# Optimization experiments

Measured on AMD Instinct MI355X. Metric: run time of the kernel, lower is better.

Reference implementation:

```python
import jax, jax.numpy as jnp
import numpy as np

B, S, D = 2, 2048, 768
H, STRIDE = 12, 8
HD = D // H  # 64


def setup_inputs() -> dict:
    key = jax.random.key(0)
    k0, k1, k2 = jax.random.split(key, 3)
    x = jax.random.normal(k0, (B, S, D), dtype=jnp.float32)
    qkv_w = jax.random.normal(k1, (3 * D, D), dtype=jnp.float32) * 0.02
    qkv_b = jnp.zeros((3 * D,), dtype=jnp.float32)
    out_w = jax.random.normal(k2, (D, D), dtype=jnp.float32) * 0.02
    out_b = jnp.zeros((D,), dtype=jnp.float32)
    return {"x": x, "qkv_w": qkv_w, "qkv_b": qkv_b, "out_w": out_w, "out_b": out_b}


def _stride_mask(S, stride, causal):
    i = jnp.arange(S)[:, None]
    j = jnp.arange(S)[None, :]
    strided = (j % stride == 0)
    if causal:
        strided = strided & (j <= i)
    # diagonal always attended; previous token attended for i > 0
    return strided | (j == i) | (j == i - 1)


def reference(x, qkv_w, qkv_b, out_w, out_b):
    Bx, Sx, Dx = x.shape
    qkv = x @ qkv_w.T + qkv_b                      # [B,S,3D]
    qkv = qkv.reshape(Bx, Sx, 3, H, HD)
    q, k, v = jnp.transpose(qkv, (2, 0, 3, 1, 4))  # each [B,H,S,HD]
    scale = HD ** -0.5
    attn = jnp.einsum('bhid,bhjd->bhij', q, k) * scale  # [B,H,S,S]
    mask = _stride_mask(Sx, STRIDE, True)          # [S,S] bool
    attn = jnp.where(mask[None, None], attn, -jnp.inf)
    a = jax.nn.softmax(attn, axis=-1)
    # every row has at least the diagonal unmasked, so no NaN rows;
    # nan_to_num kept for exact parity with the torch module
    a = jnp.nan_to_num(a, nan=0.0)
    out = jnp.einsum('bhij,bhjd->bhid', a, v)      # [B,H,S,HD]
    out = jnp.transpose(out, (0, 2, 1, 3)).reshape(Bx, Sx, Dx)
    return out @ out_w.T + out_b
```

## Files before the change

### kernel.cpp

```cpp
#include <hip/hip_runtime.h>
#include <hip/hip_bf16.h>
#include <stdint.h>

#define H_   12
#define S_   2048
#define D_   768
#define HD_  64
#define MS_  256

typedef __bf16 bf16_8 __attribute__((ext_vector_type(8)));
typedef float  f32_4  __attribute__((ext_vector_type(4)));

typedef __attribute__((address_space(1))) void* gas_ptr;
typedef __attribute__((address_space(3))) void* las_ptr;

__device__ __forceinline__ void g2l16(const void* g, void* l) {
  __builtin_amdgcn_global_load_lds((gas_ptr)g, (las_ptr)l, 16, 0, 0);
}

__device__ __forceinline__ f32_4 mfma16(bf16_8 a, bf16_8 b, f32_4 c) {
  return __builtin_amdgcn_mfma_f32_16x16x32_bf16(a, b, c, 0, 0, 0);
}

__device__ __forceinline__ bf16_8 ld8(const __hip_bfloat16* p) {
  return *reinterpret_cast<const bf16_8*>(p);
}

__global__ __launch_bounds__(256) void cvt3_f32_bf16(
    const float* __restrict__ a, const float* __restrict__ b,
    const float* __restrict__ c, __hip_bfloat16* __restrict__ out,
    int na4, int nb4) {
  const int t = blockIdx.x * 256 + threadIdx.x;
  float4 f;
  if (t < na4)            f = reinterpret_cast<const float4*>(a)[t];
  else if (t < na4 + nb4) f = reinterpret_cast<const float4*>(b)[t - na4];
  else                    f = reinterpret_cast<const float4*>(c)[t - na4 - nb4];
  union { __hip_bfloat16 h[4]; ushort4 u; } p;
  p.h[0] = __float2bfloat16(f.x);
  p.h[1] = __float2bfloat16(f.y);
  p.h[2] = __float2bfloat16(f.z);
  p.h[3] = __float2bfloat16(f.w);
  reinterpret_cast<ushort4*>(out)[t] = p.u;
}

template <int MODE, int BN>
__global__ __launch_bounds__(256, 2) void gemm_bt(
    const __hip_bfloat16* __restrict__ A, const __hip_bfloat16* __restrict__ B,
    const float* __restrict__ bias,
    __hip_bfloat16* __restrict__ O0, __hip_bfloat16* __restrict__ O1,
    __hip_bfloat16* __restrict__ O2, __hip_bfloat16* __restrict__ O3,
    __hip_bfloat16* __restrict__ O4, float* __restrict__ OF,
    int M, int N, int K) {
  constexpr int NTJ = BN / 32;
  __shared__ __bf16 sA[128 * 32];
  __shared__ __bf16 sB[BN * 32];
  const int tid  = threadIdx.x;
  const int lane = tid & 63;
  const int wv   = tid >> 6;
  const int m0 = blockIdx.y * 128;
  const int n0 = blockIdx.x * BN;
  const int wr = (wv >> 1) * 64;
  const int wc = (wv & 1) * (BN / 2);

  f32_4 acc[4][NTJ] = {};

  const __hip_bfloat16* aS = A + (size_t)(m0 + (tid >> 2)) * K + ((tid & 3) << 3);
  const __hip_bfloat16* bS = B + (size_t)(n0 + (tid >> 2)) * K + ((tid & 3) << 3);
  const size_t half = (size_t)64 * K;
  __bf16* dA  = &sA[tid * 8];
  __bf16* dA2 = &sA[tid * 8 + 2048];
  __bf16* dB  = &sB[tid * 8];
  __bf16* dB2 = &sB[tid * 8 + 2048];

  const int fr = lane & 15;
  const int kq = (lane >> 4) << 3;

  for (int k0 = 0; k0 < K; k0 += 32) {
    g2l16(aS, dA);
    g2l16(aS + half, dA2);
    g2l16(bS, dB);
    if constexpr (BN == 128) g2l16(bS + half, dB2);
    aS += 32;
    bS += 32;
    __syncthreads();
    bf16_8 af[4], bfm[NTJ];
#pragma unroll
    for (int t = 0; t < 4; ++t)
      af[t] = *reinterpret_cast<const bf16_8*>(&sA[(wr + t * 16 + fr) * 32 + kq]);
#pragma unroll
    for (int t = 0; t < NTJ; ++t)
      bfm[t] = *reinterpret_cast<const bf16_8*>(&sB[(wc + t * 16 + fr) * 32 + kq]);
#pragma unroll
    for (int ti = 0; ti < 4; ++ti)
#pragma unroll
      for (int tj = 0; tj < NTJ; ++tj)
        acc[ti][tj] = mfma16(af[ti], bfm[tj], acc[ti][tj]);
    __syncthreads();
  }

  const int crow = (lane >> 4) << 2;
  const int ccol = lane & 15;
#pragma unroll
  for (int ti = 0; ti < 4; ++ti) {
    const int gmb = m0 + wr + ti * 16 + crow;
#pragma unroll
    for (int tj = 0; tj < NTJ; ++tj) {
      const int gn = n0 + wc + tj * 16 + ccol;
      const float bv = bias[gn];
      if (MODE == 0) {
        const int t   = gn / D_;
        const int rem = gn - t * D_;
        const int hh = rem >> 6, dd = rem & 63;
        __hip_bfloat16* dst = (t == 0) ? O0 : (t == 1) ? O1 : O2;
#pragma unroll
        for (int r = 0; r < 4; ++r) {
          const int gm = gmb + r;
          const int bb = gm >> 11, ss = gm & (S_ - 1);
          const __hip_bfloat16 hv = __float2bfloat16(acc[ti][tj][r] + bv);
          dst[(((size_t)(bb * H_ + hh) << 11) + ss) * HD_ + dd] = hv;
          if (r == 0 && (gmb & 7) == 0) {
            if (t == 1)
              O4[(((size_t)(bb * H_ + hh)) * MS_ + (ss >> 3)) * HD_ + dd] = hv;
            else if (t == 2)
              O3[((size_t)(bb * H_ + hh) * HD_ + dd) * MS_ + (ss >> 3)] = hv;
          }
        }
      } else {
#pragma unroll
        for (int r = 0; r < 4; ++r)
          OF[(size_t)(gmb + r) * D_ + gn] = acc[ti][tj][r] + bv;
      }
    }
  }
}

__global__ __launch_bounds__(256) void attn_mfma(
    const __hip_bfloat16* __restrict__ Q, const __hip_bfloat16* __restrict__ Kb,
    const __hip_bfloat16* __restrict__ Ks, const __hip_bfloat16* __restrict__ Vr,
    const __hip_bfloat16* __restrict__ VsT, __hip_bfloat16* __restrict__ ctx) {
  __shared__ __bf16 pt[4][16 * 40];
  __shared__ __bf16 vb[4][32 * 64];
  const int lane = threadIdx.x & 63;
  const int wv   = threadIdx.x >> 6;
  const int task = blockIdx.x * 4 + wv;
  const int bh   = task >> 7;
  const int i0   = (task & 127) << 4;
  const int lr   = lane & 15;
  const int quad = lane >> 4;
  const float SC = 0.125f * 1.44269504088896340736f;

  const __hip_bfloat16* Kh  = Kb  + ((size_t)bh << 11) * HD_;
  const __hip_bfloat16* Ksh = Ks  + (size_t)bh * MS_ * HD_;
  const __hip_bfloat16* Vrh = Vr  + ((size_t)bh << 11) * HD_;
  const __hip_bfloat16* Vsh = VsT + (size_t)bh * HD_ * MS_;
  __bf16* ptw = pt[wv];
  __bf16* vbw = vb[wv];

  const int jbase = (i0 >= 8) ? (i0 - 8) : 0;

#pragma unroll
  for (int it = 0; it < 4; ++it) {
    const int cidx = it * 64 + lane;
    const int row = cidx >> 3, seg = cidx & 7;
    const int j  = jbase + row;
    const int jr = (j < S_) ? j : (S_ - 1);
    *reinterpret_cast<bf16_8*>(vbw + row * 64 + seg * 8) =
        ld8(Vrh + (size_t)jr * HD_ + seg * 8);
  }
  bf16_8 kb_[2][2];
#pragma unroll
  for (int t = 0; t < 2; ++t) {
    const int j  = jbase + t * 16 + lr;
    const int jr = (j < S_) ? j : (S_ - 1);
    const __hip_bfloat16* kp = Kh + (size_t)jr * HD_ + quad * 8;
    kb_[t][0] = ld8(kp);
    kb_[t][1] = ld8(kp + 32);
  }

  const __hip_bfloat16* qp = Q + (((size_t)bh << 11) + i0 + lr) * HD_ + quad * 8;
  const bf16_8 qf0 = ld8(qp);
  const bf16_8 qf1 = ld8(qp + 32);

  const __bf16 one = (__bf16)1.0f;
  const bf16_8 onesf = {one, one, one, one, one, one, one, one};

  f32_4 Lacc = {}, oacc[4];
#pragma unroll
  for (int ct = 0; ct < 4; ++ct) oacc[ct] = f32_4{0.f, 0.f, 0.f, 0.f};

  const int mmax = (i0 + 15) >> 3;
  const int nstr = (mmax >> 5) + 1;

  auto load_str = [&](int c, bf16_8 (&kf)[2][2], bf16_8 (&vf)[4]) {
    const int mb = c << 5;
#pragma unroll
    for (int t = 0; t < 2; ++t) {
      const __hip_bfloat16* kp = Ksh + (size_t)(mb + t * 16 + lr) * HD_ + quad * 8;
      kf[t][0] = ld8(kp);
      kf[t][1] = ld8(kp + 32);
    }
#pragma unroll
    for (int ct = 0; ct < 4; ++ct)
      vf[ct] = ld8(Vsh + (size_t)(ct * 16 + lr) * MS_ + mb + quad * 8);
  };

  auto softmax_pv = [&](f32_4& s0, f32_4& s1, const bf16_8 (&vf)[4]) {
#pragma unroll
    for (int r = 0; r < 4; ++r) {
      const int row = quad * 4 + r;
      ptw[row * 40 + lr]      = (__bf16)__float2bfloat16(s0[r]);
      ptw[row * 40 + 16 + lr] = (__bf16)__float2bfloat16(s1[r]);
    }
    const bf16_8 pf = *reinterpret_cast<const bf16_8*>(&ptw[lr * 40 + quad * 8]);
#pragma unroll
    for (int ct = 0; ct < 4; ++ct) oacc[ct] = mfma16(pf, vf[ct], oacc[ct]);
    Lacc = mfma16(pf, onesf, Lacc);
  };

  bf16_8 kf[2][2], vf[4], kf2[2][2], vf2[4];
  load_str(0, kf, vf);
  for (int c = 0; c < nstr; ++c) {
    const bool more = (c + 1 < nstr);
    if (more) load_str(c + 1, kf2, vf2);
    const int mb = c << 5;

    f32_4 s0 = {}, s1 = {};
    s0 = mfma16(qf0, kf[0][0], s0);
    s0 = mfma16(qf1, kf[0][1], s0);
    s1 = mfma16(qf0, kf[1][0], s1);
    s1 = mfma16(qf1, kf[1][1], s1);

#pragma unroll
    for (int r = 0; r < 4; ++r) {
      const int i = i0 + quad * 4 + r;
      const bool v0 = ((mb + lr) << 3) <= i;
      const bool v1 = ((mb + 16 + lr) << 3) <= i;
      s0[r] = v0 ? exp2f(fminf(s0[r] * SC, 63.f)) : 0.f;
      s1[r] = v1 ? exp2f(fminf(s1[r] * SC, 63.f)) : 0.f;
    }
    softmax_pv(s0, s1, vf);

    if (more) {
#pragma unroll
      for (int t = 0; t < 2; ++t) { kf[t][0] = kf2[t][0]; kf[t][1] = kf2[t][1]; }
#pragma unroll
      for (int ct = 0; ct < 4; ++ct) vf[ct] = vf2[ct];
    }
  }

  {
    f32_4 s0 = {}, s1 = {};
    s0 = mfma16(qf0, kb_[0][0], s0);
    s0 = mfma16(qf1, kb_[0][1], s0);
    s1 = mfma16(qf0, kb_[1][0], s1);
    s1 = mfma16(qf1, kb_[1][1], s1);

#pragma unroll
    for (int r = 0; r < 4; ++r) {
      const int i = i0 + quad * 4 + r;
      const int j0 = jbase + lr, j1 = jbase + 16 + lr;
      const bool v0 = (j0 == i || j0 == i - 1) && (j0 & 7);
      const bool v1 = (j1 == i || j1 == i - 1) && (j1 & 7);
      s0[r] = v0 ? exp2f(fminf(s0[r] * SC, 63.f)) : 0.f;
      s1[r] = v1 ? exp2f(fminf(s1[r] * SC, 63.f)) : 0.f;
    }

    bf16_8 vfb[4];
#pragma unroll
    for (int ct = 0; ct < 4; ++ct) {
      bf16_8 tmp;
#pragma unroll
      for (int e = 0; e < 8; ++e)
        tmp[e] = vbw[(quad * 8 + e) * 64 + ct * 16 + lr];
      vfb[ct] = tmp;
    }
    softmax_pv(s0, s1, vfb);
  }

  const int b = bh / H_;
  const int h = bh - b * H_;
  f32_4 inv;
#pragma unroll
  for (int r = 0; r < 4; ++r) inv[r] = 1.f / Lacc[r];
#pragma unroll
  for (int r = 0; r < 4; ++r) {
    const int i = i0 + quad * 4 + r;
    __hip_bfloat16* cp = ctx + ((size_t)(b * S_ + i)) * D_ + h * HD_ + lr;
#pragma unroll
    for (int ct = 0; ct < 4; ++ct)
      cp[ct * 16] = __float2bfloat16(oacc[ct][r] * inv[r]);
  }
}

extern "C" void kernel_launch(void* const* d_in, const int* in_sizes, int n_in,
                              void* d_out, int out_size, void* d_ws, size_t ws_size,
                              hipStream_t stream) {
  const float* x    = (const float*)d_in[0];
  const float* qkvw = (const float*)d_in[1];
  const float* qkvb = (const float*)d_in[2];
  const float* outw = (const float*)d_in[3];
  const float* outb = (const float*)d_in[4];
  float* out = (float*)d_out;

  const size_t NX  = (size_t)2 * S_ * D_;
  const size_t NW1 = (size_t)3 * D_ * D_;
  const size_t NW2 = (size_t)D_ * D_;
  const size_t NVS = (size_t)2 * H_ * HD_ * MS_;

  __hip_bfloat16* xb  = (__hip_bfloat16*)d_ws;
  __hip_bfloat16* w1b = xb + NX;
  __hip_bfloat16* w2b = w1b + NW1;
  __hip_bfloat16* q   = w2b + NW2;
  __hip_bfloat16* k   = q + NX;
  __hip_bfloat16* vr  = k + NX;
  __hip_bfloat16* vst = vr + NX;
  __hip_bfloat16* ks  = vst + NVS;
  __hip_bfloat16* ctx = ks + NVS;

  const int na4 = (int)(NX / 4), nb4 = (int)(NW1 / 4), nc4 = (int)(NW2 / 4);
  cvt3_f32_bf16<<<dim3((na4 + nb4 + nc4) / 256), 256, 0, stream>>>(
      x, qkvw, outw, xb, na4, nb4);

  gemm_bt<0, 128><<<dim3(2304 / 128, 4096 / 128), 256, 0, stream>>>(
      xb, w1b, qkvb, q, k, vr, vst, ks, nullptr, 4096, 2304, 768);

  attn_mfma<<<dim3(2 * H_ * S_ / 16 / 4), 256, 0, stream>>>(q, k, ks, vr, vst, ctx);

  gemm_bt<1, 64><<<dim3(768 / 64, 4096 / 128), 256, 0, stream>>>(
      ctx, w2b, outb, nullptr, nullptr, nullptr, nullptr, nullptr,
      out, 4096, 768, 768);
}
```

Before: 150.1 us.

## Fuse output projection into attention kernel with one block per 16-row tile

Attention now runs one 768-thread block per 16 query rows, with one wavefront per head. Each head writes its context slice into shared memory, and the block then computes the 16x768 output projection directly, so the ctx round-trip and the separate output GEMM launch disappear. The V tile is loaded straight into registers with scalar gathers instead of being staged through LDS. In exchange, each block streams the full W2 from global/L2 with no reuse across M tiles (only 16 rows per block). The grid also shrinks to 256 large blocks, which may hurt occupancy.

```diff
diff --git a/kernel.cpp b/kernel.cpp
--- a/kernel.cpp
+++ b/kernel.cpp
@@ -43,26 +43,23 @@
   reinterpret_cast<ushort4*>(out)[t] = p.u;
 }
 
-template <int MODE, int BN>
-__global__ __launch_bounds__(256, 2) void gemm_bt(
+__global__ __launch_bounds__(256, 2) void gemm_qkv(
     const __hip_bfloat16* __restrict__ A, const __hip_bfloat16* __restrict__ B,
     const float* __restrict__ bias,
     __hip_bfloat16* __restrict__ O0, __hip_bfloat16* __restrict__ O1,
     __hip_bfloat16* __restrict__ O2, __hip_bfloat16* __restrict__ O3,
-    __hip_bfloat16* __restrict__ O4, float* __restrict__ OF,
-    int M, int N, int K) {
-  constexpr int NTJ = BN / 32;
+    __hip_bfloat16* __restrict__ O4, int K) {
   __shared__ __bf16 sA[128 * 32];
-  __shared__ __bf16 sB[BN * 32];
+  __shared__ __bf16 sB[128 * 32];
   const int tid  = threadIdx.x;
   const int lane = tid & 63;
   const int wv   = tid >> 6;
   const int m0 = blockIdx.y * 128;
-  const int n0 = blockIdx.x * BN;
+  const int n0 = blockIdx.x * 128;
   const int wr = (wv >> 1) * 64;
-  const int wc = (wv & 1) * (BN / 2);
-
-  f32_4 acc[4][NTJ] = {};
+  const int wc = (wv & 1) * 64;
+
+  f32_4 acc[4][4] = {};
 
   const __hip_bfloat16* aS = A + (size_t)(m0 + (tid >> 2)) * K + ((tid & 3) << 3);
   const __hip_bfloat16* bS = B + (size_t)(n0 + (tid >> 2)) * K + ((tid & 3) << 3);
@@ -79,21 +76,21 @@
     g2l16(aS, dA);
     g2l16(aS + half, dA2);
     g2l16(bS, dB);
-    if constexpr (BN == 128) g2l16(bS + half, dB2);
+    g2l16(bS + half, dB2);
     aS += 32;
     bS += 32;
     __syncthreads();
-    bf16_8 af[4], bfm[NTJ];
+    bf16_8 af[4], bfm[4];
 #pragma unroll
     for (int t = 0; t < 4; ++t)
       af[t] = *reinterpret_cast<const bf16_8*>(&sA[(wr + t * 16 + fr) * 32 + kq]);
 #pragma unroll
-    for (int t = 0; t < NTJ; ++t)
+    for (int t = 0; t < 4; ++t)
       bfm[t] = *reinterpret_cast<const bf16_8*>(&sB[(wc + t * 16 + fr) * 32 + kq]);
 #pragma unroll
     for (int ti = 0; ti < 4; ++ti)
 #pragma unroll
-      for (int tj = 0; tj < NTJ; ++tj)
+      for (int tj = 0; tj < 4; ++tj)
         acc[ti][tj] = mfma16(af[ti], bfm[tj], acc[ti][tj]);
     __syncthreads();
   }
@@ -104,47 +101,43 @@
   for (int ti = 0; ti < 4; ++ti) {
     const int gmb = m0 + wr + ti * 16 + crow;
 #pragma unroll
-    for (int tj = 0; tj < NTJ; ++tj) {
+    for (int tj = 0; tj < 4; ++tj) {
       const int gn = n0 + wc + tj * 16 + ccol;
       const float bv = bias[gn];
-      if (MODE == 0) {
-        const int t   = gn / D_;
-        const int rem = gn - t * D_;
-        const int hh = rem >> 6, dd = rem & 63;
-        __hip_bfloat16* dst = (t == 0) ? O0 : (t == 1) ? O1 : O2;
-#pragma unroll
-        for (int r = 0; r < 4; ++r) {
-          const int gm = gmb + r;
-          const int bb = gm >> 11, ss = gm & (S_ - 1);
-          const __hip_bfloat16 hv = __float2bfloat16(acc[ti][tj][r] + bv);
-          dst[(((size_t)(bb * H_ + hh) << 11) + ss) * HD_ + dd] = hv;
-          if (r == 0 && (gmb & 7) == 0) {
-            if (t == 1)
-              O4[(((size_t)(bb * H_ + hh)) * MS_ + (ss >> 3)) * HD_ + dd] = hv;
-            else if (t == 2)
-              O3[((size_t)(bb * H_ + hh) * HD_ + dd) * MS_ + (ss >> 3)] = hv;
-          }
+      const int t   = gn / D_;
+      const int rem = gn - t * D_;
+      const int hh = rem >> 6, dd = rem & 63;
+      __hip_bfloat16* dst = (t == 0) ? O0 : (t == 1) ? O1 : O2;
+#pragma unroll
+      for (int r = 0; r < 4; ++r) {
+        const int gm = gmb + r;
+        const int bb = gm >> 11, ss = gm & (S_ - 1);
+        const __hip_bfloat16 hv = __float2bfloat16(acc[ti][tj][r] + bv);
+        dst[(((size_t)(bb * H_ + hh) << 11) + ss) * HD_ + dd] = hv;
+        if (r == 0 && (gmb & 7) == 0) {
+          if (t == 1)
+            O4[(((size_t)(bb * H_ + hh)) * MS_ + (ss >> 3)) * HD_ + dd] = hv;
+          else if (t == 2)
+            O3[((size_t)(bb * H_ + hh) * HD_ + dd) * MS_ + (ss >> 3)] = hv;
         }
-      } else {
-#pragma unroll
-        for (int r = 0; r < 4; ++r)
-          OF[(size_t)(gmb + r) * D_ + gn] = acc[ti][tj][r] + bv;
       }
     }
   }
 }
 
-__global__ __launch_bounds__(256) void attn_mfma(
+__global__ __launch_bounds__(768) void attn_out(
     const __hip_bfloat16* __restrict__ Q, const __hip_bfloat16* __restrict__ Kb,
     const __hip_bfloat16* __restrict__ Ks, const __hip_bfloat16* __restrict__ Vr,
-    const __hip_bfloat16* __restrict__ VsT, __hip_bfloat16* __restrict__ ctx) {
-  __shared__ __bf16 pt[4][16 * 40];
-  __shared__ __bf16 vb[4][32 * 64];
+    const __hip_bfloat16* __restrict__ VsT, const __hip_bfloat16* __restrict__ W2,
+    const float* __restrict__ b2, float* __restrict__ out) {
+  __shared__ __bf16 pt[12][16 * 40];
+  __shared__ __bf16 cx[16][776];
   const int lane = threadIdx.x & 63;
-  const int wv   = threadIdx.x >> 6;
-  const int task = blockIdx.x * 4 + wv;
-  const int bh   = task >> 7;
+  const int h    = threadIdx.x >> 6;
+  const int task = blockIdx.x;
+  const int b    = task >> 7;
   const int i0   = (task & 127) << 4;
+  const int bh   = b * H_ + h;
   const int lr   = lane & 15;
   const int quad = lane >> 4;
   const float SC = 0.125f * 1.44269504088896340736f;
@@ -153,20 +146,20 @@
   const __hip_bfloat16* Ksh = Ks  + (size_t)bh * MS_ * HD_;
   const __hip_bfloat16* Vrh = Vr  + ((size_t)bh << 11) * HD_;
   const __hip_bfloat16* Vsh = VsT + (size_t)bh * HD_ * MS_;
-  __bf16* ptw = pt[wv];
-  __bf16* vbw = vb[wv];
+  __bf16* ptw = pt[h];
 
   const int jbase = (i0 >= 8) ? (i0 - 8) : 0;
 
-#pragma unroll
-  for (int it = 0; it < 4; ++it) {
-    const int cidx = it * 64 + lane;
-    const int row = cidx >> 3, seg = cidx & 7;
-    const int j  = jbase + row;
-    const int jr = (j < S_) ? j : (S_ - 1);
-    *reinterpret_cast<bf16_8*>(vbw + row * 64 + seg * 8) =
-        ld8(Vrh + (size_t)jr * HD_ + seg * 8);
-  }
+  const __bf16* Vrb = reinterpret_cast<const __bf16*>(Vrh);
+  bf16_8 vfb[4];
+#pragma unroll
+  for (int ct = 0; ct < 4; ++ct)
+#pragma unroll
+    for (int e = 0; e < 8; ++e) {
+      const int j  = jbase + quad * 8 + e;
+      const int jr = (j < S_) ? j : (S_ - 1);
+      vfb[ct][e] = Vrb[(size_t)jr * HD_ + ct * 16 + lr];
+    }
   bf16_8 kb_[2][2];
 #pragma unroll
   for (int t = 0; t < 2; ++t) {
@@ -264,31 +257,39 @@
       s0[r] = v0 ? exp2f(fminf(s0[r] * SC, 63.f)) : 0.f;
       s1[r] = v1 ? exp2f(fminf(s1[r] * SC, 63.f)) : 0.f;
     }
-
-    bf16_8 vfb[4];
-#pragma unroll
-    for (int ct = 0; ct < 4; ++ct) {
-      bf16_8 tmp;
-#pragma unroll
-      for (int e = 0; e < 8; ++e)
-        tmp[e] = vbw[(quad * 8 + e) * 64 + ct * 16 + lr];
-      vfb[ct] = tmp;
-    }
     softmax_pv(s0, s1, vfb);
   }
 
-  const int b = bh / H_;
-  const int h = bh - b * H_;
   f32_4 inv;
 #pragma unroll
   for (int r = 0; r < 4; ++r) inv[r] = 1.f / Lacc[r];
 #pragma unroll
-  for (int r = 0; r < 4; ++r) {
-    const int i = i0 + quad * 4 + r;
-    __hip_bfloat16* cp = ctx + ((size_t)(b * S_ + i)) * D_ + h * HD_ + lr;
-#pragma unroll
-    for (int ct = 0; ct < 4; ++ct)
-      cp[ct * 16] = __float2bfloat16(oacc[ct][r] * inv[r]);
+  for (int ct = 0; ct < 4; ++ct)
+#pragma unroll
+    for (int r = 0; r < 4; ++r)
+      cx[quad * 4 + r][h * 64 + ct * 16 + lr] =
+          (__bf16)__float2bfloat16(oacc[ct][r] * inv[r]);
+  __syncthreads();
+
+  f32_4 oa[4] = {};
+  for (int ks = 0; ks < 24; ++ks) {
+    const bf16_8 af = *reinterpret_cast<const bf16_8*>(&cx[lr][ks * 32 + quad * 8]);
+#pragma unroll
+    for (int t = 0; t < 4; ++t) {
+      const int n = h * 64 + t * 16 + lr;
+      const bf16_8 bf = ld8(W2 + (size_t)n * D_ + ks * 32 + quad * 8);
+      oa[t] = mfma16(af, bf, oa[t]);
+    }
+  }
+#pragma unroll
+  for (int t = 0; t < 4; ++t) {
+    const int n = h * 64 + t * 16 + lr;
+    const float bv = b2[n];
+#pragma unroll
+    for (int r = 0; r < 4; ++r) {
+      const int m = i0 + quad * 4 + r;
+      out[(size_t)(b * S_ + m) * D_ + n] = oa[t][r] + bv;
+    }
   }
 }
 
@@ -315,18 +316,14 @@
   __hip_bfloat16* vr  = k + NX;
   __hip_bfloat16* vst = vr + NX;
   __hip_bfloat16* ks  = vst + NVS;
-  __hip_bfloat16* ctx = ks + NVS;
 
   const int na4 = (int)(NX / 4), nb4 = (int)(NW1 / 4), nc4 = (int)(NW2 / 4);
   cvt3_f32_bf16<<<dim3((na4 + nb4 + nc4) / 256), 256, 0, stream>>>(
       x, qkvw, outw, xb, na4, nb4);
 
-  gemm_bt<0, 128><<<dim3(2304 / 128, 4096 / 128), 256, 0, stream>>>(
-      xb, w1b, qkvb, q, k, vr, vst, ks, nullptr, 4096, 2304, 768);
-
-  attn_mfma<<<dim3(2 * H_ * S_ / 16 / 4), 256, 0, stream>>>(q, k, ks, vr, vst, ctx);
-
-  gemm_bt<1, 64><<<dim3(768 / 64, 4096 / 128), 256, 0, stream>>>(
-      ctx, w2b, outb, nullptr, nullptr, nullptr, nullptr, nullptr,
-      out, 4096, 768, 768);
-}
+  gemm_qkv<<<dim3(2304 / 128, 4096 / 128), 256, 0, stream>>>(
+      xb, w1b, qkvb, q, k, vr, vst, ks, 768);
+
+  attn_out<<<dim3(2 * S_ / 16), 768, 0, stream>>>(
+      q, k, ks, vr, vst, w2b, outb, out);
+}
```

Result: slower. 167.9 us (+11.9%).

## Split each attention query tile across two waves and reduce partials through LDS

Applied to the files above, without the earlier changes.

Each 16-row query tile is now handled by two wavefronts. They take alternating strided key chunks, and one of them also does the local-band block. The partial outputs and row sums are combined through shared memory after a block barrier. The grid doubles, and the local V band is gathered with scalar global loads instead of being staged through LDS. This is meant to shorten the serial chunk loop per wave and raise parallelism, which matters most for late query tiles with many strided keys. The cost is an added __syncthreads, an LDS reduction, and less coalesced V loads.

```diff
diff --git a/kernel.cpp b/kernel.cpp
--- a/kernel.cpp
+++ b/kernel.cpp
@@ -139,10 +139,12 @@
     const __hip_bfloat16* __restrict__ Ks, const __hip_bfloat16* __restrict__ Vr,
     const __hip_bfloat16* __restrict__ VsT, __hip_bfloat16* __restrict__ ctx) {
   __shared__ __bf16 pt[4][16 * 40];
-  __shared__ __bf16 vb[4][32 * 64];
+  __shared__ float ox[2][64][20];
   const int lane = threadIdx.x & 63;
   const int wv   = threadIdx.x >> 6;
-  const int task = blockIdx.x * 4 + wv;
+  const int tp   = wv >> 1;
+  const int part = wv & 1;
+  const int task = blockIdx.x * 2 + tp;
   const int bh   = task >> 7;
   const int i0   = (task & 127) << 4;
   const int lr   = lane & 15;
@@ -154,27 +156,28 @@
   const __hip_bfloat16* Vrh = Vr  + ((size_t)bh << 11) * HD_;
   const __hip_bfloat16* Vsh = VsT + (size_t)bh * HD_ * MS_;
   __bf16* ptw = pt[wv];
-  __bf16* vbw = vb[wv];
 
   const int jbase = (i0 >= 8) ? (i0 - 8) : 0;
 
-#pragma unroll
-  for (int it = 0; it < 4; ++it) {
-    const int cidx = it * 64 + lane;
-    const int row = cidx >> 3, seg = cidx & 7;
-    const int j  = jbase + row;
-    const int jr = (j < S_) ? j : (S_ - 1);
-    *reinterpret_cast<bf16_8*>(vbw + row * 64 + seg * 8) =
-        ld8(Vrh + (size_t)jr * HD_ + seg * 8);
-  }
-  bf16_8 kb_[2][2];
-#pragma unroll
-  for (int t = 0; t < 2; ++t) {
-    const int j  = jbase + t * 16 + lr;
-    const int jr = (j < S_) ? j : (S_ - 1);
-    const __hip_bfloat16* kp = Kh + (size_t)jr * HD_ + quad * 8;
-    kb_[t][0] = ld8(kp);
-    kb_[t][1] = ld8(kp + 32);
+  bf16_8 vfb[4], kb_[2][2];
+  if (part) {
+    const __bf16* Vrb = reinterpret_cast<const __bf16*>(Vrh);
+#pragma unroll
+    for (int ct = 0; ct < 4; ++ct)
+#pragma unroll
+      for (int e = 0; e < 8; ++e) {
+        const int j  = jbase + quad * 8 + e;
+        const int jr = (j < S_) ? j : (S_ - 1);
+        vfb[ct][e] = Vrb[(size_t)jr * HD_ + ct * 16 + lr];
+      }
+#pragma unroll
+    for (int t = 0; t < 2; ++t) {
+      const int j  = jbase + t * 16 + lr;
+      const int jr = (j < S_) ? j : (S_ - 1);
+      const __hip_bfloat16* kp = Kh + (size_t)jr * HD_ + quad * 8;
+      kb_[t][0] = ld8(kp);
+      kb_[t][1] = ld8(kp + 32);
+    }
   }
 
   const __hip_bfloat16* qp = Q + (((size_t)bh << 11) + i0 + lr) * HD_ + quad * 8;
@@ -218,10 +221,10 @@
   };
 
   bf16_8 kf[2][2], vf[4], kf2[2][2], vf2[4];
-  load_str(0, kf, vf);
-  for (int c = 0; c < nstr; ++c) {
-    const bool more = (c + 1 < nstr);
-    if (more) load_str(c + 1, kf2, vf2);
+  if (part < nstr) load_str(part, kf, vf);
+  for (int c = part; c < nstr; c += 2) {
+    const bool more = (c + 2 < nstr);
+    if (more) load_str(c + 2, kf2, vf2);
     const int mb = c << 5;
 
     f32_4 s0 = {}, s1 = {};
@@ -248,7 +251,7 @@
     }
   }
 
-  {
+  if (part) {
     f32_4 s0 = {}, s1 = {};
     s0 = mfma16(qf0, kb_[0][0], s0);
     s0 = mfma16(qf1, kb_[0][1], s0);
@@ -264,31 +267,38 @@
       s0[r] = v0 ? exp2f(fminf(s0[r] * SC, 63.f)) : 0.f;
       s1[r] = v1 ? exp2f(fminf(s1[r] * SC, 63.f)) : 0.f;
     }
-
-    bf16_8 vfb[4];
-#pragma unroll
-    for (int ct = 0; ct < 4; ++ct) {
-      bf16_8 tmp;
-#pragma unroll
-      for (int e = 0; e < 8; ++e)
-        tmp[e] = vbw[(quad * 8 + e) * 64 + ct * 16 + lr];
-      vfb[ct] = tmp;
-    }
     softmax_pv(s0, s1, vfb);
-  }
-
-  const int b = bh / H_;
-  const int h = bh - b * H_;
-  f32_4 inv;
-#pragma unroll
-  for (int r = 0; r < 4; ++r) inv[r] = 1.f / Lacc[r];
-#pragma unroll
-  for (int r = 0; r < 4; ++r) {
-    const int i = i0 + quad * 4 + r;
-    __hip_bfloat16* cp = ctx + ((size_t)(b * S_ + i)) * D_ + h * HD_ + lr;
+
 #pragma unroll
     for (int ct = 0; ct < 4; ++ct)
-      cp[ct * 16] = __float2bfloat16(oacc[ct][r] * inv[r]);
+#pragma unroll
+      for (int r = 0; r < 4; ++r) ox[tp][lane][ct * 4 + r] = oacc[ct][r];
+#pragma unroll
+    for (int r = 0; r < 4; ++r) ox[tp][lane][16 + r] = Lacc[r];
+  }
+  __syncthreads();
+
+  if (!part) {
+#pragma unroll
+    for (int ct = 0; ct < 4; ++ct)
+#pragma unroll
+      for (int r = 0; r < 4; ++r) oacc[ct][r] += ox[tp][lane][ct * 4 + r];
+#pragma unroll
+    for (int r = 0; r < 4; ++r) Lacc[r] += ox[tp][lane][16 + r];
+
+    const int b = bh / H_;
+    const int h = bh - b * H_;
+    f32_4 inv;
+#pragma unroll
+    for (int r = 0; r < 4; ++r) inv[r] = 1.f / Lacc[r];
+#pragma unroll
+    for (int r = 0; r < 4; ++r) {
+      const int i = i0 + quad * 4 + r;
+      __hip_bfloat16* cp = ctx + ((size_t)(b * S_ + i)) * D_ + h * HD_ + lr;
+#pragma unroll
+      for (int ct = 0; ct < 4; ++ct)
+        cp[ct * 16] = __float2bfloat16(oacc[ct][r] * inv[r]);
+    }
   }
 }
 
@@ -324,7 +334,8 @@
   gemm_bt<0, 128><<<dim3(2304 / 128, 4096 / 128), 256, 0, stream>>>(
       xb, w1b, qkvb, q, k, vr, vst, ks, nullptr, 4096, 2304, 768);
 
-  attn_mfma<<<dim3(2 * H_ * S_ / 16 / 4), 256, 0, stream>>>(q, k, ks, vr, vst, ctx);
+  attn_mfma<<<dim3(2 * H_ * S_ / 16 / 2), 256, 0, stream>>>(
+      q, k, ks, vr, vst, ctx);
 
   gemm_bt<1, 64><<<dim3(768 / 64, 4096 / 128), 256, 0, stream>>>(
       ctx, w2b, outb, nullptr, nullptr, nullptr, nullptr, nullptr,
```

After: 148.5 us (median of 2 runs). No clear change (-1.0%).
